# Kernel optimization log

Measured on AMD Instinct MI355X. Metric: run time of the kernel, lower is better.

## Reference

```python
import jax, jax.numpy as jnp
import numpy as np

N = 20000      # nodes
E = 320000     # edges (before self-loops)
DIN = 128      # input_dim
HID = 256      # hidden_dim
HEADS = 8
C = HID // HEADS  # per-head channels = 32
G = 16         # graphs in batch
OUT = 2
EPS = 1e-5


def setup_inputs() -> dict:
    key = jax.random.key(0)
    ks = jax.random.split(key, 24)

    def lin(k, fan_in, fan_out):
        return jax.random.normal(k, (fan_in, fan_out), jnp.float32) / np.float32(np.sqrt(fan_in))

    inp = {
        "x": jax.random.normal(ks[0], (N, DIN), jnp.float32),
        "edge_index": jax.random.randint(ks[1], (2, E), 0, N, jnp.int64),
        "batch": jnp.sort(jax.random.randint(ks[2], (N,), 0, G, jnp.int64)),
        # encoder
        "enc_w": lin(ks[3], DIN, HID), "enc_b": jnp.zeros((HID,), jnp.float32),
        # gat1 (GATv2: lin_l, lin_r, att, out bias)
        "g1_wl": lin(ks[4], HID, HID), "g1_bl": jnp.zeros((HID,), jnp.float32),
        "g1_wr": lin(ks[5], HID, HID), "g1_br": jnp.zeros((HID,), jnp.float32),
        "g1_att": jax.random.normal(ks[6], (HEADS, C), jnp.float32) / np.float32(np.sqrt(C)),
        "g1_bias": jnp.zeros((HID,), jnp.float32),
        # gat2
        "g2_wl": lin(ks[7], HID, HID), "g2_bl": jnp.zeros((HID,), jnp.float32),
        "g2_wr": lin(ks[8], HID, HID), "g2_br": jnp.zeros((HID,), jnp.float32),
        "g2_att": jax.random.normal(ks[9], (HEADS, C), jnp.float32) / np.float32(np.sqrt(C)),
        "g2_bias": jnp.zeros((HID,), jnp.float32),
        # layernorm
        "ln_g": jnp.ones((HID,), jnp.float32), "ln_b": jnp.zeros((HID,), jnp.float32),
        # head MLP
        "h1_w": lin(ks[10], HID, HID // 2), "h1_b": jnp.zeros((HID // 2,), jnp.float32),
        "h2_w": lin(ks[11], HID // 2, OUT), "h2_b": jnp.zeros((OUT,), jnp.float32),
    }
    return inp


def _gatv2(x, src, dst, wl, bl, wr, br, att, bias, n):
    # GATv2Conv (PyG semantics, eval mode so dropout is identity)
    h, c = att.shape
    xl = (x @ wl + bl).reshape(n, h, c)   # source transform
    xr = (x @ wr + br).reshape(n, h, c)   # target transform
    e = jax.nn.leaky_relu(xl[src] + xr[dst], 0.2)       # [E, H, C]
    score = jnp.einsum('ehc,hc->eh', e, att)            # [E, H]
    smax = jax.ops.segment_max(score, dst, num_segments=n)
    ex = jnp.exp(score - smax[dst])
    denom = jax.ops.segment_sum(ex, dst, num_segments=n)
    alpha = ex / denom[dst]                             # segment softmax over incoming edges
    out = jax.ops.segment_sum(alpha[:, :, None] * xl[src], dst, num_segments=n)
    return out.reshape(n, h * c) + bias


def _layernorm(x, g, b):
    mu = jnp.mean(x, axis=-1, keepdims=True)
    var = jnp.mean(jnp.square(x - mu), axis=-1, keepdims=True)
    return (x - mu) * jax.lax.rsqrt(var + EPS) * g + b


def reference(x, edge_index, batch, enc_w, enc_b,
              g1_wl, g1_bl, g1_wr, g1_br, g1_att, g1_bias,
              g2_wl, g2_bl, g2_wr, g2_br, g2_att, g2_bias,
              ln_g, ln_b, h1_w, h1_b, h2_w, h2_b):
    n = x.shape[0]
    # PyG GATv2Conv default add_self_loops=True
    loops = jnp.arange(n, dtype=edge_index.dtype)
    src = jnp.concatenate([edge_index[0], loops])
    dst = jnp.concatenate([edge_index[1], loops])

    h = jax.nn.relu(x @ enc_w + enc_b)
    h = jax.nn.relu(_gatv2(h, src, dst, g1_wl, g1_bl, g1_wr, g1_br, g1_att, g1_bias, n))
    h = _layernorm(h, ln_g, ln_b)
    h = jax.nn.relu(_gatv2(h, src, dst, g2_wl, g2_bl, g2_wr, g2_br, g2_att, g2_bias, n))

    # global_mean_pool over graph ids
    sums = jax.ops.segment_sum(h, batch, num_segments=G)
    counts = jax.ops.segment_sum(jnp.ones((n,), h.dtype), batch, num_segments=G)
    pooled = sums / jnp.maximum(counts, 1.0)[:, None]

    out = jax.nn.relu(pooled @ h1_w + h1_b) @ h2_w + h2_b
    return out
```

## Files before the change

### kernel.cpp

```cpp
#include <hip/hip_runtime.h>
#include <hip/hip_fp16.h>

#define HIDDIM 256
#define NHEADS 8
#define SCORE_SHIFT 4.0f
#define XSTR 512

struct __attribute__((aligned(8))) half4s { __half2 a, b; };

typedef _Float16 f16x8 __attribute__((ext_vector_type(8)));
typedef float f32x4 __attribute__((ext_vector_type(4)));

__global__ __launch_bounds__(256) void cvt_f2h(
    const float* __restrict__ in, __half* __restrict__ out, int n) {
  const int i = blockIdx.x * 256 + threadIdx.x;
  if (i < n) out[i] = __float2half(in[i]);
}

__global__ __launch_bounds__(256) void cvt_transpose(
    const float* __restrict__ in, __half* __restrict__ out, int K, int N) {
  const int idx = blockIdx.x * 256 + threadIdx.x;
  if (idx >= K * N) return;
  const int n = idx / K, k = idx - n * K;
  out[idx] = __float2half(in[(size_t)k * N + n]);
}

__global__ __launch_bounds__(256) void cvt_transpose4(
    const float* __restrict__ w0, const float* __restrict__ w1,
    const float* __restrict__ w2, const float* __restrict__ w3,
    __half* __restrict__ o0, __half* __restrict__ o1,
    __half* __restrict__ o2, __half* __restrict__ o3) {
  const float* in; __half* out;
  switch (blockIdx.y) {
    case 0: in = w0; out = o0; break;
    case 1: in = w1; out = o1; break;
    case 2: in = w2; out = o2; break;
    default: in = w3; out = o3; break;
  }
  const int idx = blockIdx.x * 256 + threadIdx.x;
  if (idx >= HIDDIM * HIDDIM) return;
  const int n = idx / HIDDIM, k = idx - n * HIDDIM;
  out[idx] = __float2half(in[(size_t)k * HIDDIM + n]);
}

__global__ __launch_bounds__(256) void concat_biases(
    const float* __restrict__ bl0, const float* __restrict__ br0,
    const float* __restrict__ bl1, const float* __restrict__ br1,
    float* __restrict__ o0, float* __restrict__ o1) {
  const int i = blockIdx.x * 256 + threadIdx.x;
  if (i >= 2 * XSTR) return;
  const int layer = i >> 9, pos = i & (XSTR - 1);
  const float* bl = layer ? bl1 : bl0;
  const float* br = layer ? br1 : br0;
  float v = (pos < HIDDIM) ? bl[pos] : br[pos - HIDDIM];
  (layer ? o1 : o0)[pos] = v;
}

template <int RELU, int KT>
__global__ __launch_bounds__(256) void gemm_mfma(
    const _Float16* __restrict__ A, const _Float16* __restrict__ Wt,
    const float* __restrict__ bias, _Float16* __restrict__ C,
    int M, int N) {
  const int wv = threadIdx.x >> 6;
  const int lane = threadIdx.x & 63;
  const int bn = blockIdx.x * 128;
  const int bm = blockIdx.y * 128 + wv * 32;
  const int fr = lane & 15;
  const int kb = lane >> 4;

  int ar0 = bm + fr;      if (ar0 >= M) ar0 = M - 1;
  int ar1 = bm + 16 + fr; if (ar1 >= M) ar1 = M - 1;
  const _Float16* ap0 = A + (size_t)ar0 * KT + kb * 8;
  const _Float16* ap1 = A + (size_t)ar1 * KT + kb * 8;
  const _Float16* bp  = Wt + (size_t)(bn + fr) * KT + kb * 8;

  f32x4 acc[2][8] = {};
  #pragma unroll
  for (int k0 = 0; k0 < KT; k0 += 32) {
    const f16x8 a0 = *(const f16x8*)(ap0 + k0);
    const f16x8 a1 = *(const f16x8*)(ap1 + k0);
    #pragma unroll
    for (int nt = 0; nt < 8; ++nt) {
      const f16x8 b = *(const f16x8*)(bp + (size_t)nt * 16 * KT + k0);
      acc[0][nt] = __builtin_amdgcn_mfma_f32_16x16x32_f16(a0, b, acc[0][nt], 0, 0, 0);
      acc[1][nt] = __builtin_amdgcn_mfma_f32_16x16x32_f16(a1, b, acc[1][nt], 0, 0, 0);
    }
  }
  #pragma unroll
  for (int g = 0; g < 2; ++g) {
    #pragma unroll
    for (int r = 0; r < 4; ++r) {
      const int row = bm + g * 16 + (lane >> 4) * 4 + r;
      if (row >= M) continue;
      #pragma unroll
      for (int nt = 0; nt < 8; ++nt) {
        const int col = bn + nt * 16 + fr;
        float v = acc[g][nt][r] + bias[col];
        if (RELU && v < 0.f) v = 0.f;
        C[(size_t)row * N + col] = (_Float16)v;
      }
    }
  }
}

__global__ __launch_bounds__(256) void count_deg(
    const int* __restrict__ ei, int* __restrict__ deg, int E, int Nn) {
  const int t = blockIdx.x * blockDim.x + threadIdx.x;
  const int ET = E + Nn;
  if (t >= ET) return;
  const int dst = (t < E) ? ei[E + t] : (t - E);
  atomicAdd(&deg[dst], 1);
}

__global__ __launch_bounds__(1024) void scan_deg(
    const int* __restrict__ deg, int* __restrict__ rowptr, int Nn) {
  __shared__ int wsum[16];
  __shared__ int carry_s;
  const int tid = threadIdx.x;
  const int wid = tid >> 6, lane = tid & 63;
  if (tid == 0) { carry_s = 0; rowptr[0] = 0; }
  __syncthreads();
  for (int base = 0; base < Nn; base += 1024) {
    const int i = base + tid;
    int s = (i < Nn) ? deg[i] : 0;
    #pragma unroll
    for (int off = 1; off < 64; off <<= 1) {
      int t = __shfl_up(s, off);
      if (lane >= off) s += t;
    }
    if (lane == 63) wsum[wid] = s;
    __syncthreads();
    if (wid == 0 && lane < 16) {
      int ws = wsum[lane];
      #pragma unroll
      for (int off = 1; off < 16; off <<= 1) {
        int t = __shfl_up(ws, off);
        if (lane >= off) ws += t;
      }
      wsum[lane] = ws;
    }
    __syncthreads();
    const int prefix = (wid > 0 ? wsum[wid - 1] : 0) + carry_s;
    if (i < Nn) rowptr[i + 1] = s + prefix;
    __syncthreads();
    if (tid == 0) carry_s += wsum[15];
    __syncthreads();
  }
}

__global__ __launch_bounds__(256) void fill_csr(
    const int* __restrict__ ei, const int* __restrict__ rowptr,
    int* __restrict__ cursor, int* __restrict__ csr, int E, int Nn) {
  const int t = blockIdx.x * blockDim.x + threadIdx.x;
  const int ET = E + Nn;
  if (t >= ET) return;
  int src, dst;
  if (t < E) { src = ei[t]; dst = ei[E + t]; }
  else { src = t - E; dst = t - E; }
  const int pos = atomicAdd(&cursor[dst], 1);
  csr[rowptr[dst] + pos] = src;
}

__global__ __launch_bounds__(256) void graph_ranges(
    const int* __restrict__ batch, int* __restrict__ gstart, int Nn, int G) {
  const int n = blockIdx.x * 256 + threadIdx.x;
  if (n > Nn) return;
  if (n == 0) {
    for (int g = 0; g <= batch[0]; ++g) gstart[g] = 0;
  } else if (n == Nn) {
    for (int g = batch[Nn - 1] + 1; g <= G; ++g) gstart[g] = Nn;
  } else {
    const int b = batch[n], bp = batch[n - 1];
    for (int g = bp + 1; g <= b; ++g) gstart[g] = n;
  }
}

template <int MODE>
__global__ __launch_bounds__(256) void node_gat(
    const __half* __restrict__ xlr,
    const int* __restrict__ rowptr, const int* __restrict__ csr,
    const float* __restrict__ att, const float* __restrict__ bias,
    const float* __restrict__ lng, const float* __restrict__ lnb,
    __half* __restrict__ outp, int Nn) {
  int n = (int)((blockIdx.x * (size_t)blockDim.x + threadIdx.x) >> 6);
  const int lane = threadIdx.x & 63;
  if (n >= Nn) return;
  n = __builtin_amdgcn_readfirstlane(n);
  const int r0 = rowptr[n], r1 = rowptr[n + 1];
  const int jm = r1 - 1;
  const half4s* __restrict__ xlv = (const half4s*)xlr;
  float4 xr4;
  {
    const half4s xrh = xlv[(size_t)n * (XSTR / 4) + 64 + lane];
    const float2 f01 = __half22float2(xrh.a);
    const float2 f23 = __half22float2(xrh.b);
    xr4 = make_float4(f01.x, f01.y, f23.x, f23.y);
  }
  const float4 at4 = *(const float4*)(att + lane * 4);
  float4 acc = make_float4(0.f, 0.f, 0.f, 0.f);
  float den = 0.f;

  for (int j0 = r0; j0 <= jm; j0 += 8) {
    half4s r[8];
    #pragma unroll
    for (int k = 0; k < 8; ++k) {
      int j = j0 + k; j = j <= jm ? j : jm;
      r[k] = xlv[(size_t)csr[j] * (XSTR / 4) + lane];
    }
    float4 a[8];
    float s[8];
    #pragma unroll
    for (int k = 0; k < 8; ++k) {
      const float2 f01 = __half22float2(r[k].a);
      const float2 f23 = __half22float2(r[k].b);
      a[k] = make_float4(f01.x, f01.y, f23.x, f23.y);
      float v, ss;
      v = a[k].x + xr4.x; v = v >= 0.f ? v : 0.2f * v; ss = v * at4.x;
      v = a[k].y + xr4.y; v = v >= 0.f ? v : 0.2f * v; ss = fmaf(v, at4.y, ss);
      v = a[k].z + xr4.z; v = v >= 0.f ? v : 0.2f * v; ss = fmaf(v, at4.z, ss);
      v = a[k].w + xr4.w; v = v >= 0.f ? v : 0.2f * v; ss = fmaf(v, at4.w, ss);
      s[k] = ss;
    }
    #pragma unroll
    for (int k = 0; k < 8; ++k) {
      s[k] += __shfl_xor(s[k], 1);
      s[k] += __shfl_xor(s[k], 2);
      s[k] += __shfl_xor(s[k], 4);
    }
    float w[8];
    #pragma unroll
    for (int k = 0; k < 8; ++k)
      w[k] = (j0 + k <= jm) ? __expf(s[k] - SCORE_SHIFT) : 0.f;
    #pragma unroll
    for (int k = 0; k < 8; ++k) {
      acc.x = fmaf(w[k], a[k].x, acc.x);
      acc.y = fmaf(w[k], a[k].y, acc.y);
      acc.z = fmaf(w[k], a[k].z, acc.z);
      acc.w = fmaf(w[k], a[k].w, acc.w);
      den += w[k];
    }
  }
  const float inv_d = 1.f / den;
  const float4 bb = *(const float4*)(bias + lane * 4);
  float t0 = fmaf(acc.x, inv_d, bb.x); t0 = t0 > 0.f ? t0 : 0.f;
  float t1 = fmaf(acc.y, inv_d, bb.y); t1 = t1 > 0.f ? t1 : 0.f;
  float t2 = fmaf(acc.z, inv_d, bb.z); t2 = t2 > 0.f ? t2 : 0.f;
  float t3 = fmaf(acc.w, inv_d, bb.w); t3 = t3 > 0.f ? t3 : 0.f;

  if (MODE == 0) {
    float s = t0 + t1 + t2 + t3;
    #pragma unroll
    for (int mm = 1; mm < 64; mm <<= 1) s += __shfl_xor(s, mm);
    const float mu = s * (1.f / HIDDIM);
    const float d0 = t0 - mu, d1 = t1 - mu, d2 = t2 - mu, d3 = t3 - mu;
    float q = d0 * d0 + d1 * d1 + d2 * d2 + d3 * d3;
    #pragma unroll
    for (int mm = 1; mm < 64; mm <<= 1) q += __shfl_xor(q, mm);
    const float inv = rsqrtf(q * (1.f / HIDDIM) + 1e-5f);
    const float4 g4 = *(const float4*)(lng + lane * 4);
    const float4 b4 = *(const float4*)(lnb + lane * 4);
    half4s ho;
    ho.a = __floats2half2_rn(d0 * inv * g4.x + b4.x, d1 * inv * g4.y + b4.y);
    ho.b = __floats2half2_rn(d2 * inv * g4.z + b4.z, d3 * inv * g4.w + b4.w);
    *((half4s*)outp + (size_t)n * (HIDDIM / 4) + lane) = ho;
  } else {
    half4s ho;
    ho.a = __floats2half2_rn(t0, t1);
    ho.b = __floats2half2_rn(t2, t3);
    *((half4s*)outp + (size_t)n * (HIDDIM / 4) + lane) = ho;
  }
}

__global__ __launch_bounds__(256) void pool_kernel(
    const __half* __restrict__ tbuf, const int* __restrict__ gstart,
    float* __restrict__ pooled) {
  const int g = blockIdx.x, rc = blockIdx.y, ch = threadIdx.x;
  const int n0 = gstart[g], n1 = gstart[g + 1];
  float acc = 0.f;
  for (int n = n0 + rc; n < n1; n += 8)
    acc += __half2float(tbuf[(size_t)n * HIDDIM + ch]);
  atomicAdd(&pooled[g * HIDDIM + ch], acc);
}

__global__ __launch_bounds__(256) void head_kernel(
    const float* __restrict__ pooled, const int* __restrict__ gstart,
    const float* __restrict__ h1w, const float* __restrict__ h1b,
    const float* __restrict__ h2w, const float* __restrict__ h2b,
    float* __restrict__ out, int H1, int OUT) {
  const int g = blockIdx.x;
  __shared__ float P[HIDDIM];
  __shared__ float Hh[128];
  const int tid = threadIdx.x;
  float cnt = (float)(gstart[g + 1] - gstart[g]);
  if (cnt < 1.f) cnt = 1.f;
  P[tid] = pooled[g * HIDDIM + tid] / cnt;
  __syncthreads();
  if (tid < H1) {
    float s = h1b[tid];
    for (int k = 0; k < HIDDIM; ++k) s = fmaf(P[k], h1w[k * H1 + tid], s);
    Hh[tid] = s > 0.f ? s : 0.f;
  }
  __syncthreads();
  if (tid < OUT) {
    float s = h2b[tid];
    for (int k = 0; k < H1; ++k) s = fmaf(Hh[k], h2w[k * OUT + tid], s);
    out[g * OUT + tid] = s;
  }
}

extern "C" void kernel_launch(void* const* d_in, const int* in_sizes, int n_in,
                              void* d_out, int out_size, void* d_ws, size_t ws_size,
                              hipStream_t stream) {
  const float* x = (const float*)d_in[0];
  const int* ei = (const int*)d_in[1];
  const int* batch = (const int*)d_in[2];
  const float* enc_w = (const float*)d_in[3];
  const float* enc_b = (const float*)d_in[4];
  const float* g_wl[2] = {(const float*)d_in[5], (const float*)d_in[11]};
  const float* g_bl[2] = {(const float*)d_in[6], (const float*)d_in[12]};
  const float* g_wr[2] = {(const float*)d_in[7], (const float*)d_in[13]};
  const float* g_br[2] = {(const float*)d_in[8], (const float*)d_in[14]};
  const float* g_att[2] = {(const float*)d_in[9], (const float*)d_in[15]};
  const float* g_bias[2] = {(const float*)d_in[10], (const float*)d_in[16]};
  const float* ln_g = (const float*)d_in[17];
  const float* ln_b = (const float*)d_in[18];
  const float* h1_w = (const float*)d_in[19];
  const float* h1_b = (const float*)d_in[20];
  const float* h2_w = (const float*)d_in[21];
  const float* h2_b = (const float*)d_in[22];
  float* out = (float*)d_out;

  const int N = in_sizes[2];
  const int E = in_sizes[1] / 2;
  const int DIN = in_sizes[0] / N;
  const int ET = E + N;
  const int H1 = in_sizes[20];
  const int OUT = in_sizes[22];
  const int G = out_size / OUT;

  char* base = (char*)d_ws;
  const size_t NH = (size_t)N * HIDDIM;
  __half* h16  = (__half*)base;
  __half* xlr  = h16 + NH;
  __half* tbuf = xlr + NH * 2;
  __half* x16  = tbuf + NH;
  __half* wtE  = x16 + (size_t)N * DIN;
  __half* wtC0 = wtE + (size_t)HIDDIM * DIN;
  __half* wtC1 = wtC0 + (size_t)XSTR * HIDDIM;
  float* biasC0 = (float*)(wtC1 + (size_t)XSTR * HIDDIM);
  float* biasC1 = biasC0 + XSTR;
  float* pooled = biasC1 + XSTR;
  int* gstart = (int*)(pooled + (size_t)G * HIDDIM);
  int* deg    = gstart + (G + 1);
  int* rowptr = deg + N;
  int* cursor = rowptr + (N + 1);
  int* csr    = cursor + N;

  const dim3 blk(256);
  const int eb = (ET + 255) / 256;
  const int nb = (N + 3) / 4;
  const dim3 enc_grid(HIDDIM / 128, (N + 127) / 128);
  const dim3 cmb_grid(XSTR / 128, (N + 127) / 128);

  hipMemsetAsync(deg, 0, (size_t)N * sizeof(int), stream);
  hipMemsetAsync(cursor, 0, (size_t)N * sizeof(int), stream);
  hipMemsetAsync(pooled, 0, (size_t)G * HIDDIM * sizeof(float), stream);
  count_deg<<<eb, blk, 0, stream>>>(ei, deg, E, N);
  scan_deg<<<1, 1024, 0, stream>>>(deg, rowptr, N);
  fill_csr<<<eb, blk, 0, stream>>>(ei, rowptr, cursor, csr, E, N);
  graph_ranges<<<(N + 256) / 256, blk, 0, stream>>>(batch, gstart, N, G);

  cvt_f2h<<<(N * DIN + 255) / 256, blk, 0, stream>>>(x, x16, N * DIN);
  cvt_transpose<<<(DIN * HIDDIM + 255) / 256, blk, 0, stream>>>(enc_w, wtE, DIN, HIDDIM);
  cvt_transpose4<<<dim3((HIDDIM * HIDDIM + 255) / 256, 4), blk, 0, stream>>>(
      g_wl[0], g_wr[0], g_wl[1], g_wr[1],
      wtC0, wtC0 + (size_t)HIDDIM * HIDDIM, wtC1, wtC1 + (size_t)HIDDIM * HIDDIM);
  concat_biases<<<(2 * XSTR + 255) / 256, blk, 0, stream>>>(
      g_bl[0], g_br[0], g_bl[1], g_br[1], biasC0, biasC1);

  gemm_mfma<1, 128><<<enc_grid, blk, 0, stream>>>(
      (const _Float16*)x16, (const _Float16*)wtE, enc_b, (_Float16*)h16, N, HIDDIM);

  for (int L = 0; L < 2; ++L) {
    const __half* wtC = (L == 0) ? wtC0 : wtC1;
    const float* bC = (L == 0) ? biasC0 : biasC1;
    gemm_mfma<0, 256><<<cmb_grid, blk, 0, stream>>>(
        (const _Float16*)h16, (const _Float16*)wtC, bC, (_Float16*)xlr, N, XSTR);
    if (L == 0) {
      node_gat<0><<<nb, blk, 0, stream>>>(xlr, rowptr, csr, g_att[0], g_bias[0],
                                          ln_g, ln_b, h16, N);
    } else {
      node_gat<1><<<nb, blk, 0, stream>>>(xlr, rowptr, csr, g_att[1], g_bias[1],
                                          nullptr, nullptr, tbuf, N);
      pool_kernel<<<dim3(G, 8), blk, 0, stream>>>(tbuf, gstart, pooled);
    }
  }
  head_kernel<<<G, blk, 0, stream>>>(pooled, gstart, h1_w, h1_b, h2_w, h2_b, out, H1, OUT);
}
```

Measured before the change: 296.4 us.

## Stage GEMM weight tiles in LDS, single-pass degree scan, merge memsets

The MFMA GEMM now loads each 128x32 weight tile cooperatively into padded shared memory once per k-step, so the four waves no longer each fetch it from global memory. This costs two barriers per k-step. The degree scan is rewritten as a single pass in which each thread scans a contiguous chunk in registers, replacing a loop of 1024-element rounds full of barriers. The deg and cursor buffers are placed next to each other so one memset clears both.

Result: faster. 245.1 us (-17.3%).

```diff
diff --git a/kernel.cpp b/kernel.cpp
--- a/kernel.cpp
+++ b/kernel.cpp
@@ -5,6 +5,7 @@
 #define NHEADS 8
 #define SCORE_SHIFT 4.0f
 #define XSTR 512
+#define BPAD 40
 
 struct __attribute__((aligned(8))) half4s { __half2 a, b; };
 
@@ -61,8 +62,10 @@
     const _Float16* __restrict__ A, const _Float16* __restrict__ Wt,
     const float* __restrict__ bias, _Float16* __restrict__ C,
     int M, int N) {
-  const int wv = threadIdx.x >> 6;
-  const int lane = threadIdx.x & 63;
+  __shared__ _Float16 Bs[128 * BPAD];
+  const int tid = threadIdx.x;
+  const int wv = tid >> 6;
+  const int lane = tid & 63;
   const int bn = blockIdx.x * 128;
   const int bm = blockIdx.y * 128 + wv * 32;
   const int fr = lane & 15;
@@ -72,16 +75,24 @@
   int ar1 = bm + 16 + fr; if (ar1 >= M) ar1 = M - 1;
   const _Float16* ap0 = A + (size_t)ar0 * KT + kb * 8;
   const _Float16* ap1 = A + (size_t)ar1 * KT + kb * 8;
-  const _Float16* bp  = Wt + (size_t)(bn + fr) * KT + kb * 8;
+
+  const int sc = tid >> 2;
+  const int sch = (tid & 3) * 8;
 
   f32x4 acc[2][8] = {};
   #pragma unroll
   for (int k0 = 0; k0 < KT; k0 += 32) {
     const f16x8 a0 = *(const f16x8*)(ap0 + k0);
     const f16x8 a1 = *(const f16x8*)(ap1 + k0);
+    const f16x8 s0 = *(const f16x8*)(Wt + (size_t)(bn + sc) * KT + k0 + sch);
+    const f16x8 s1 = *(const f16x8*)(Wt + (size_t)(bn + 64 + sc) * KT + k0 + sch);
+    __syncthreads();
+    *(f16x8*)(Bs + sc * BPAD + sch) = s0;
+    *(f16x8*)(Bs + (64 + sc) * BPAD + sch) = s1;
+    __syncthreads();
     #pragma unroll
     for (int nt = 0; nt < 8; ++nt) {
-      const f16x8 b = *(const f16x8*)(bp + (size_t)nt * 16 * KT + k0);
+      const f16x8 b = *(const f16x8*)(Bs + (nt * 16 + fr) * BPAD + kb * 8);
       acc[0][nt] = __builtin_amdgcn_mfma_f32_16x16x32_f16(a0, b, acc[0][nt], 0, 0, 0);
       acc[1][nt] = __builtin_amdgcn_mfma_f32_16x16x32_f16(a1, b, acc[1][nt], 0, 0, 0);
     }
@@ -114,38 +125,50 @@
 
 __global__ __launch_bounds__(1024) void scan_deg(
     const int* __restrict__ deg, int* __restrict__ rowptr, int Nn) {
-  __shared__ int wsum[16];
-  __shared__ int carry_s;
   const int tid = threadIdx.x;
   const int wid = tid >> 6, lane = tid & 63;
-  if (tid == 0) { carry_s = 0; rowptr[0] = 0; }
+  const int CH = (Nn + 1023) >> 10;
+  const int base = tid * CH;
+  int s[32];
+  int run = 0;
+  #pragma unroll
+  for (int i = 0; i < 32; ++i) {
+    if (i < CH) {
+      const int idx = base + i;
+      const int v = (idx < Nn) ? deg[idx] : 0;
+      run += v;
+    }
+    s[i] = run;
+  }
+  int tot = run;
+  #pragma unroll
+  for (int off = 1; off < 64; off <<= 1) {
+    int t = __shfl_up(tot, off);
+    if (lane >= off) tot += t;
+  }
+  __shared__ int wsum[16];
+  __shared__ int wpre[16];
+  if (lane == 63) wsum[wid] = tot;
   __syncthreads();
-  for (int base = 0; base < Nn; base += 1024) {
-    const int i = base + tid;
-    int s = (i < Nn) ? deg[i] : 0;
-    #pragma unroll
-    for (int off = 1; off < 64; off <<= 1) {
-      int t = __shfl_up(s, off);
-      if (lane >= off) s += t;
-    }
-    if (lane == 63) wsum[wid] = s;
-    __syncthreads();
-    if (wid == 0 && lane < 16) {
-      int ws = wsum[lane];
-      #pragma unroll
-      for (int off = 1; off < 16; off <<= 1) {
-        int t = __shfl_up(ws, off);
-        if (lane >= off) ws += t;
-      }
-      wsum[lane] = ws;
-    }
-    __syncthreads();
-    const int prefix = (wid > 0 ? wsum[wid - 1] : 0) + carry_s;
-    if (i < Nn) rowptr[i + 1] = s + prefix;
-    __syncthreads();
-    if (tid == 0) carry_s += wsum[15];
-    __syncthreads();
-  }
+  if (tid < 16) {
+    int ws = wsum[tid];
+    #pragma unroll
+    for (int off = 1; off < 16; off <<= 1) {
+      int t = __shfl_up(ws, off);
+      if (tid >= off) ws += t;
+    }
+    wpre[tid] = ws;
+  }
+  __syncthreads();
+  const int excl = (wid ? wpre[wid - 1] : 0) + (tot - run);
+  #pragma unroll
+  for (int i = 0; i < 32; ++i) {
+    if (i < CH) {
+      const int idx = base + i;
+      if (idx < Nn) rowptr[idx + 1] = excl + s[i];
+    }
+  }
+  if (tid == 0) rowptr[0] = 0;
 }
 
 __global__ __launch_bounds__(256) void fill_csr(
@@ -352,9 +375,9 @@
   float* pooled = biasC1 + XSTR;
   int* gstart = (int*)(pooled + (size_t)G * HIDDIM);
   int* deg    = gstart + (G + 1);
-  int* rowptr = deg + N;
-  int* cursor = rowptr + (N + 1);
-  int* csr    = cursor + N;
+  int* cursor = deg + N;
+  int* rowptr = cursor + N;
+  int* csr    = rowptr + (N + 1);
 
   const dim3 blk(256);
   const int eb = (ET + 255) / 256;
@@ -362,8 +385,7 @@
   const dim3 enc_grid(HIDDIM / 128, (N + 127) / 128);
   const dim3 cmb_grid(XSTR / 128, (N + 127) / 128);
 
-  hipMemsetAsync(deg, 0, (size_t)N * sizeof(int), stream);
-  hipMemsetAsync(cursor, 0, (size_t)N * sizeof(int), stream);
+  hipMemsetAsync(deg, 0, (size_t)2 * N * sizeof(int), stream);
   hipMemsetAsync(pooled, 0, (size_t)G * HIDDIM * sizeof(float), stream);
   count_deg<<<eb, blk, 0, stream>>>(ei, deg, E, N);
   scan_deg<<<1, 1024, 0, stream>>>(deg, rowptr, N);
```
